# Kernel optimization log

Hardware: AMD Instinct MI355X
Metric: run time of the kernel (lower is better)

## Reference

```python
import math
import jax, jax.numpy as jnp
import numpy as np

BLOCK = 256
LAYER_IDX = 5
NUM_HIDDEN_LAYERS = 32


def get_slopes(head_dim):
    equ = lambda x: 1 / 2 ** (8 / x)
    log2 = math.log2(head_dim)
    if log2.is_integer():
        return [equ(head_dim) ** i for i in range(1, head_dim + 1)]
    lower = 2 ** math.floor(log2)
    upper = 2 ** math.ceil(log2)
    ls = get_slopes(lower)
    us = get_slopes(upper)
    return ls + us[::2][: head_dim - lower]


def setup_inputs() -> dict:
    key = jax.random.key(0)
    k1, k2, k3 = jax.random.split(key, 3)
    B, H, S, D = 2, 64, 4096, 64
    q = jax.random.normal(k1, (B, H, S, D), dtype=jnp.float32)
    k = jax.random.normal(k2, (B, H, S, D), dtype=jnp.float32)
    v = jax.random.normal(k3, (B, H, S, D), dtype=jnp.float32)
    mask = jnp.ones((B, S), dtype=jnp.int32)
    return {"query_states": q, "key_states": k, "value_states": v, "attention_mask": mask}


def _lightning_attention(q, k, v, attention_mask):
    B, H, S, D = q.shape
    E = v.shape[-1]
    # mask padded positions in values
    v = v * attention_mask[:, None, :, None].astype(v.dtype)

    # per-head decay slopes, scaled by layer depth (note: H == D by construction)
    slopes = np.asarray(get_slopes(D), dtype=np.float32)
    slopes = slopes * (1.0 - LAYER_IDX / (NUM_HIDDEN_LAYERS - 1) + 1e-05)
    slope = jnp.asarray(slopes)[:, None, None]  # [H, 1, 1]

    arr = jnp.arange(1, BLOCK + 1, dtype=jnp.float32)
    q_decay = jnp.exp(-slope * arr[:, None])            # [H, BLOCK, 1]
    k_decay = jnp.exp(-slope * (BLOCK - arr)[:, None])  # [H, BLOCK, 1]
    idx = arr[:, None] - arr[None, :]                   # [BLOCK, BLOCK]
    s_idx = slope * idx[None]                           # [H, BLOCK, BLOCK] (slope [H,1,1] broadcasts)
    diag_decay = jnp.exp(jnp.where(idx[None] >= 0, -s_idx, -jnp.inf))  # [H, BLOCK, BLOCK]
    block_decay = jnp.exp(-slope * BLOCK)               # [H, 1, 1]

    nb = S // BLOCK
    qb = q.reshape(B, H, nb, BLOCK, D).transpose(2, 0, 1, 3, 4)  # [nb, B, H, BLOCK, D]
    kb = k.reshape(B, H, nb, BLOCK, D).transpose(2, 0, 1, 3, 4)
    vb = v.reshape(B, H, nb, BLOCK, E).transpose(2, 0, 1, 3, 4)

    def step(kv, blk):
        qi, ki, vi = blk  # each [B, H, BLOCK, D/E]
        # inter-block: decayed query reads recurrent kv state
        o_inter = jnp.einsum('bhmd,bhde->bhme', qi * q_decay, kv)
        # intra-block: causal decayed attention within the block
        qk = jnp.einsum('bhmd,bhnd->bhmn', qi, ki) * diag_decay
        o_intra = jnp.einsum('bhmn,bhne->bhme', qk, vi)
        # update recurrent state
        kv_new = block_decay * kv + jnp.einsum('bhmd,bhme->bhde', ki * k_decay, vi)
        return kv_new, o_inter + o_intra

    kv0 = jnp.zeros((B, H, D, E), dtype=jnp.float32)
    _, outs = jax.lax.scan(step, kv0, (qb, kb, vb))  # outs: [nb, B, H, BLOCK, E]
    out = outs.transpose(1, 2, 0, 3, 4).reshape(B, H, S, E)
    return out


def reference(query_states, key_states, value_states, attention_mask):
    return _lightning_attention(query_states, key_states, value_states, attention_mask)
```

## Files before the change

### kernel.cpp

```cpp
#include <hip/hip_runtime.h>

typedef __attribute__((ext_vector_type(4))) float f4;
typedef __attribute__((ext_vector_type(4))) float f32x4;
typedef __attribute__((ext_vector_type(8))) short short8;
typedef __attribute__((ext_vector_type(4))) short short4v;
typedef __attribute__((ext_vector_type(4))) unsigned int uint4v;

#define S_  4096
#define NB_ 16
#define SLOPE_SCALE 0.838719677419355f

__device__ __forceinline__ float slope_for_head(int h) {
    return exp2f(-(float)(h + 1) * 0.125f) * SLOPE_SCALE;
}

__device__ __forceinline__ short f2bf(float f) {
    unsigned u = __float_as_uint(f);
    u += 0x7FFFu + ((u >> 16) & 1u);
    return (short)(u >> 16);
}

__global__ __launch_bounds__(256, 4) void phase1_kvblocks(
    const float* __restrict__ k, const float* __restrict__ v,
    const int* __restrict__ mask, float* __restrict__ kvt,
    short* __restrict__ vt)
{
    __shared__ float ks[64][68];
    __shared__ float vs[64][68];
    const int j  = blockIdx.x;
    const int bh = blockIdx.y;
    const int b  = bh >> 6;
    const int h  = bh & 63;
    const int t  = threadIdx.x;
    const float slope = slope_for_head(h);
    const int e  = t >> 2;
    const int dg = (t & 3) << 4;

    const f32x4 zf = {0.f, 0.f, 0.f, 0.f};
    f4 acc[4];
    acc[0] = zf; acc[1] = zf; acc[2] = zf; acc[3] = zf;

    const long long tilebase = ((long long)bh * S_ + j * 256) * 64;

    for (int c = 0; c < 4; ++c) {
        for (int i = 0; i < 4; ++i) {
            int fi  = t + i * 256;
            int row = fi >> 4;
            int col = (fi & 15) << 2;
            long long g = tilebase + (long long)(c * 64 + row) * 64 + col;
            *(f4*)&ks[row][col] = *(const f4*)(k + g);
            f4 vv = *(const f4*)(v + g);
            float mv = (float)mask[b * S_ + j * 256 + c * 64 + row];
            vv *= mv;
            *(f4*)&vs[row][col] = vv;
        }
        __syncthreads();

        for (int n = 0; n < 64; ++n) {
            float kd = __expf(-slope * (float)(255 - (c * 64 + n)));
            float a  = vs[n][e] * kd;
            const f4* krow = (const f4*)&ks[n][dg];
            acc[0] += a * krow[0];
            acc[1] += a * krow[1];
            acc[2] += a * krow[2];
            acc[3] += a * krow[3];
        }

        {
            int nb = (t & 3) << 4;
            unsigned w[8];
            for (int i = 0; i < 8; ++i) {
                unsigned lo = (unsigned short)f2bf(vs[nb + 2 * i][e]);
                unsigned hi = (unsigned short)f2bf(vs[nb + 2 * i + 1][e]);
                w[i] = lo | (hi << 16);
            }
            long long g = ((long long)(bh * 64 + e)) * S_ + j * 256 + c * 64 + nb;
            uint4v* dst = (uint4v*)(vt + g);
            uint4v w0 = {w[0], w[1], w[2], w[3]};
            uint4v w1 = {w[4], w[5], w[6], w[7]};
            dst[0] = w0;
            dst[1] = w1;
        }
        __syncthreads();
    }

    float* o = kvt + ((long long)(bh * NB_ + j)) * 4096 + e * 64 + dg;
    *(f4*)(o + 0)  = acc[0];
    *(f4*)(o + 4)  = acc[1];
    *(f4*)(o + 8)  = acc[2];
    *(f4*)(o + 12) = acc[3];
}

__global__ __launch_bounds__(256) void phase2_scan(float* __restrict__ kvt)
{
    const int bh = blockIdx.x;
    const int h  = bh & 63;
    const int t  = threadIdx.x;
    const float slope = slope_for_head(h);
    const float bd = __expf(-slope * 256.0f);

    const f32x4 zf = {0.f, 0.f, 0.f, 0.f};
    f4 st[4];
    st[0] = zf; st[1] = zf; st[2] = zf; st[3] = zf;

    f4* base = (f4*)(kvt + (long long)bh * NB_ * 4096);
    for (int j = 0; j < NB_; ++j) {
        f4* p = base + j * 1024;
        for (int i = 0; i < 4; ++i) {
            f4 tmp = p[t + i * 256];
            p[t + i * 256] = st[i];
            st[i] = st[i] * bd + tmp;
        }
    }
}

__global__ __launch_bounds__(256, 2) void phase3_output(
    const float* __restrict__ q, const float* __restrict__ k,
    const float* __restrict__ kvt, const short* __restrict__ vt,
    float* __restrict__ out)
{
    __shared__ short P[4][64 * 56];
    const int j    = blockIdx.x;
    const int bh   = blockIdx.y;
    const int h    = bh & 63;
    const int tid  = threadIdx.x;
    const int wave = tid >> 6;
    const int lane = tid & 63;
    const int quad = lane >> 4;
    const int l16  = lane & 15;
    const int wrole  = (wave + j) & 3;
    const float slope = slope_for_head(h);
    const int mwbase = wrole << 6;

    const long long rowbase = (long long)bh * S_ + j * 256 + mwbase;

    short8 qf[4][2];
    for (int mt = 0; mt < 4; ++mt) {
        const float* qp = q + (rowbase + mt * 16 + l16) * 64 + quad * 8;
        for (int ks = 0; ks < 2; ++ks) {
            f4 a = *(const f4*)(qp + ks * 32);
            f4 b = *(const f4*)(qp + ks * 32 + 4);
            short8 f;
            f[0] = f2bf(a.x); f[1] = f2bf(a.y); f[2] = f2bf(a.z); f[3] = f2bf(a.w);
            f[4] = f2bf(b.x); f[5] = f2bf(b.y); f[6] = f2bf(b.z); f[7] = f2bf(b.w);
            qf[mt][ks] = f;
        }
    }

    const f32x4 zf = {0.f, 0.f, 0.f, 0.f};
    f32x4 of[4][4];
    for (int et = 0; et < 4; ++et)
        for (int mt = 0; mt < 4; ++mt) of[et][mt] = zf;

    const float* kvp = kvt + ((long long)(bh * NB_ + j) << 12);
    for (int et = 0; et < 4; ++et) {
        for (int ks = 0; ks < 2; ++ks) {
            const float* p = kvp + (et * 16 + l16) * 64 + ks * 32 + quad * 8;
            f4 a = *(const f4*)(p);
            f4 b = *(const f4*)(p + 4);
            short8 af;
            af[0] = f2bf(a.x); af[1] = f2bf(a.y); af[2] = f2bf(a.z); af[3] = f2bf(a.w);
            af[4] = f2bf(b.x); af[5] = f2bf(b.y); af[6] = f2bf(b.z); af[7] = f2bf(b.w);
            for (int mt = 0; mt < 4; ++mt)
                of[et][mt] = __builtin_amdgcn_mfma_f32_16x16x32_bf16(
                    af, qf[mt][ks], of[et][mt], 0, 0, 0);
        }
    }
    for (int mt = 0; mt < 4; ++mt) {
        float qd = __expf(-slope * (float)(mwbase + mt * 16 + l16 + 1));
        for (int et = 0; et < 4; ++et) of[et][mt] *= qd;
    }

    const float er1 = __expf(slope);
    const float er2 = er1 * er1;
    const float er3 = er2 * er1;
    short* Pw = &P[wave][0];
    const int nchunks = (mwbase >> 5) + 2;

    for (int c = 0; c < nchunks; ++c) {
        const int nbase = c << 5;

        short8 kf[2][2];
        for (int nt = 0; nt < 2; ++nt) {
            const float* kp = k + ((long long)bh * S_ + j * 256 + nbase + nt * 16 + l16) * 64 + quad * 8;
            for (int ks = 0; ks < 2; ++ks) {
                f4 a = *(const f4*)(kp + ks * 32);
                f4 b = *(const f4*)(kp + ks * 32 + 4);
                short8 f;
                f[0] = f2bf(a.x); f[1] = f2bf(a.y); f[2] = f2bf(a.z); f[3] = f2bf(a.w);
                f[4] = f2bf(b.x); f[5] = f2bf(b.y); f[6] = f2bf(b.z); f[7] = f2bf(b.w);
                kf[nt][ks] = f;
            }
        }

        f32x4 sf[2][4];
        for (int nt = 0; nt < 2; ++nt)
            for (int mt = 0; mt < 4; ++mt) sf[nt][mt] = zf;
        for (int nt = 0; nt < 2; ++nt)
            for (int ks = 0; ks < 2; ++ks)
                for (int mt = 0; mt < 4; ++mt)
                    sf[nt][mt] = __builtin_amdgcn_mfma_f32_16x16x32_bf16(
                        kf[nt][ks], qf[mt][ks], sf[nt][mt], 0, 0, 0);

        for (int nt = 0; nt < 2; ++nt) {
            for (int mt = 0; mt < 4; ++mt) {
                int n0 = nbase + nt * 16 + quad * 4;
                int m  = mwbase + mt * 16 + l16;
                float ddb = __expf(-slope * (float)(m - n0));
                f32x4 s = sf[nt][mt];
                float v0 = (m >= n0)     ? s[0] * ddb       : 0.f;
                float v1 = (m >= n0 + 1) ? s[1] * ddb * er1 : 0.f;
                float v2 = (m >= n0 + 2) ? s[2] * ddb * er2 : 0.f;
                float v3 = (m >= n0 + 3) ? s[3] * ddb * er3 : 0.f;
                short4v pk = {f2bf(v0), f2bf(v1), f2bf(v2), f2bf(v3)};
                *(short4v*)&Pw[(mt * 16 + l16) * 56 + nt * 16 + quad * 4] = pk;
            }
        }
        asm volatile("s_waitcnt lgkmcnt(0)" ::: "memory");

        short8 pb[4];
        for (int mt = 0; mt < 4; ++mt)
            pb[mt] = *(const short8*)&Pw[(mt * 16 + l16) * 56 + quad * 8];
        short8 va[4];
        for (int et = 0; et < 4; ++et)
            va[et] = *(const short8*)(vt + ((long long)(bh * 64 + et * 16 + l16)) * S_
                                         + j * 256 + nbase + quad * 8);

        for (int et = 0; et < 4; ++et)
            for (int mt = 0; mt < 4; ++mt)
                of[et][mt] = __builtin_amdgcn_mfma_f32_16x16x32_bf16(
                    va[et], pb[mt], of[et][mt], 0, 0, 0);
    }

    for (int mt = 0; mt < 4; ++mt) {
        float* orow = out + (rowbase + mt * 16 + l16) * 64;
        for (int et = 0; et < 4; ++et) {
            f4 o = {of[et][mt][0], of[et][mt][1], of[et][mt][2], of[et][mt][3]};
            *(f4*)(orow + et * 16 + quad * 4) = o;
        }
    }
}

extern "C" void kernel_launch(void* const* d_in, const int* in_sizes, int n_in,
                              void* d_out, int out_size, void* d_ws, size_t ws_size,
                              hipStream_t stream) {
    const float* q    = (const float*)d_in[0];
    const float* k    = (const float*)d_in[1];
    const float* v    = (const float*)d_in[2];
    const int*   mask = (const int*)d_in[3];
    float* kvt = (float*)d_ws;
    short* vt  = (short*)((char*)d_ws + (size_t)128 * 16 * 4096 * 4);
    float* out = (float*)d_out;

    phase1_kvblocks<<<dim3(16, 128), 256, 0, stream>>>(k, v, mask, kvt, vt);
    phase2_scan<<<128, 256, 0, stream>>>(kvt);
    phase3_output<<<dim3(16, 128), 256, 0, stream>>>(q, k, kvt, vt, out);
}
```

Baseline: 552.1 us.

## Use MFMA for block KV state, precompute bf16 K, and widen scan grid

```diff
diff --git a/kernel.cpp b/kernel.cpp
--- a/kernel.cpp
+++ b/kernel.cpp
@@ -4,11 +4,11 @@
 typedef __attribute__((ext_vector_type(4))) float f32x4;
 typedef __attribute__((ext_vector_type(8))) short short8;
 typedef __attribute__((ext_vector_type(4))) short short4v;
-typedef __attribute__((ext_vector_type(4))) unsigned int uint4v;
 
 #define S_  4096
 #define NB_ 16
 #define SLOPE_SCALE 0.838719677419355f
+#define ST1 136
 
 __device__ __forceinline__ float slope_for_head(int h) {
     return exp2f(-(float)(h + 1) * 0.125f) * SLOPE_SCALE;
@@ -23,99 +23,111 @@
 __global__ __launch_bounds__(256, 4) void phase1_kvblocks(
     const float* __restrict__ k, const float* __restrict__ v,
     const int* __restrict__ mask, float* __restrict__ kvt,
-    short* __restrict__ vt)
+    short* __restrict__ vt, short* __restrict__ kb)
 {
-    __shared__ float ks[64][68];
-    __shared__ float vs[64][68];
-    const int j  = blockIdx.x;
-    const int bh = blockIdx.y;
-    const int b  = bh >> 6;
-    const int h  = bh & 63;
-    const int t  = threadIdx.x;
+    __shared__ short kts[64 * ST1];
+    __shared__ short vts[64 * ST1];
+    const int j    = blockIdx.x;
+    const int bh   = blockIdx.y;
+    const int b    = bh >> 6;
+    const int h    = bh & 63;
+    const int t    = threadIdx.x;
+    const int wave = t >> 6;
+    const int lane = t & 63;
+    const int quad = lane >> 4;
+    const int l16  = lane & 15;
     const float slope = slope_for_head(h);
-    const int e  = t >> 2;
-    const int dg = (t & 3) << 4;
+
+    const long long tilebase = ((long long)bh * S_ + j * 256) * 64;
 
     const f32x4 zf = {0.f, 0.f, 0.f, 0.f};
-    f4 acc[4];
+    f32x4 acc[4];
     acc[0] = zf; acc[1] = zf; acc[2] = zf; acc[3] = zf;
 
-    const long long tilebase = ((long long)bh * S_ + j * 256) * 64;
-
-    for (int c = 0; c < 4; ++c) {
+    for (int half = 0; half < 2; ++half) {
+        const int noff = half * 128;
+
         for (int i = 0; i < 4; ++i) {
-            int fi  = t + i * 256;
-            int row = fi >> 4;
-            int col = (fi & 15) << 2;
-            long long g = tilebase + (long long)(c * 64 + row) * 64 + col;
-            *(f4*)&ks[row][col] = *(const f4*)(k + g);
-            f4 vv = *(const f4*)(v + g);
-            float mv = (float)mask[b * S_ + j * 256 + c * 64 + row];
-            vv *= mv;
-            *(f4*)&vs[row][col] = vv;
+            int u  = t + i * 256;
+            int np = u >> 4;
+            int dg = (u & 15) << 2;
+            int nl = np << 1;
+            int na = noff + nl;
+            long long g0 = tilebase + (long long)na * 64 + dg;
+
+            f4 k0 = *(const f4*)(k + g0);
+            f4 k1 = *(const f4*)(k + g0 + 64);
+            f4 v0 = *(const f4*)(v + g0);
+            f4 v1 = *(const f4*)(v + g0 + 64);
+            float m0 = (float)mask[b * S_ + j * 256 + na];
+            float m1 = (float)mask[b * S_ + j * 256 + na + 1];
+            v0 *= m0; v1 *= m1;
+            float kd0 = __expf(-slope * (float)(255 - na));
+            float kd1 = __expf(-slope * (float)(254 - na));
+
+            short4v kb0 = {f2bf(k0.x), f2bf(k0.y), f2bf(k0.z), f2bf(k0.w)};
+            short4v kb1 = {f2bf(k1.x), f2bf(k1.y), f2bf(k1.z), f2bf(k1.w)};
+            *(short4v*)(kb + g0) = kb0;
+            *(short4v*)(kb + g0 + 64) = kb1;
+
+            f4 kda = k0 * kd0;
+            f4 kdb = k1 * kd1;
+            for (int x = 0; x < 4; ++x) {
+                unsigned kw = (unsigned)(unsigned short)f2bf(kda[x]) |
+                              ((unsigned)(unsigned short)f2bf(kdb[x]) << 16);
+                unsigned vw = (unsigned)(unsigned short)f2bf(v0[x]) |
+                              ((unsigned)(unsigned short)f2bf(v1[x]) << 16);
+                *(unsigned*)&kts[(dg + x) * ST1 + nl] = kw;
+                *(unsigned*)&vts[(dg + x) * ST1 + nl] = vw;
+            }
         }
         __syncthreads();
 
-        for (int n = 0; n < 64; ++n) {
-            float kd = __expf(-slope * (float)(255 - (c * 64 + n)));
-            float a  = vs[n][e] * kd;
-            const f4* krow = (const f4*)&ks[n][dg];
-            acc[0] += a * krow[0];
-            acc[1] += a * krow[1];
-            acc[2] += a * krow[2];
-            acc[3] += a * krow[3];
+        for (int ks = 0; ks < 4; ++ks) {
+            int n0 = ks * 32;
+            short8 af = *(const short8*)&vts[(wave * 16 + l16) * ST1 + n0 + quad * 8];
+            for (int dt = 0; dt < 4; ++dt) {
+                short8 bf = *(const short8*)&kts[(dt * 16 + l16) * ST1 + n0 + quad * 8];
+                acc[dt] = __builtin_amdgcn_mfma_f32_16x16x32_bf16(af, bf, acc[dt], 0, 0, 0);
+            }
         }
 
         {
-            int nb = (t & 3) << 4;
-            unsigned w[8];
-            for (int i = 0; i < 8; ++i) {
-                unsigned lo = (unsigned short)f2bf(vs[nb + 2 * i][e]);
-                unsigned hi = (unsigned short)f2bf(vs[nb + 2 * i + 1][e]);
-                w[i] = lo | (hi << 16);
-            }
-            long long g = ((long long)(bh * 64 + e)) * S_ + j * 256 + c * 64 + nb;
-            uint4v* dst = (uint4v*)(vt + g);
-            uint4v w0 = {w[0], w[1], w[2], w[3]};
-            uint4v w1 = {w[4], w[5], w[6], w[7]};
-            dst[0] = w0;
-            dst[1] = w1;
+            int e  = t >> 2;
+            int ng = (t & 3) << 5;
+            long long gv = (long long)(bh * 64 + e) * S_ + j * 256 + noff + ng;
+            for (int x = 0; x < 4; ++x)
+                *(short8*)(vt + gv + x * 8) = *(const short8*)&vts[e * ST1 + ng + x * 8];
         }
         __syncthreads();
     }
 
-    float* o = kvt + ((long long)(bh * NB_ + j)) * 4096 + e * 64 + dg;
-    *(f4*)(o + 0)  = acc[0];
-    *(f4*)(o + 4)  = acc[1];
-    *(f4*)(o + 8)  = acc[2];
-    *(f4*)(o + 12) = acc[3];
+    float* o = kvt + ((long long)(bh * NB_ + j)) * 4096;
+    for (int dt = 0; dt < 4; ++dt)
+        for (int r = 0; r < 4; ++r)
+            o[(wave * 16 + quad * 4 + r) * 64 + dt * 16 + l16] = acc[dt][r];
 }
 
 __global__ __launch_bounds__(256) void phase2_scan(float* __restrict__ kvt)
 {
-    const int bh = blockIdx.x;
-    const int h  = bh & 63;
-    const int t  = threadIdx.x;
-    const float slope = slope_for_head(h);
-    const float bd = __expf(-slope * 256.0f);
-
-    const f32x4 zf = {0.f, 0.f, 0.f, 0.f};
-    f4 st[4];
-    st[0] = zf; st[1] = zf; st[2] = zf; st[3] = zf;
-
-    f4* base = (f4*)(kvt + (long long)bh * NB_ * 4096);
+    const int g    = blockIdx.x;
+    const int bh   = g >> 2;
+    const int part = g & 3;
+    const int h    = bh & 63;
+    const float bd = __expf(-slope_for_head(h) * 256.0f);
+
+    f32x4 st = {0.f, 0.f, 0.f, 0.f};
+    f4* base = (f4*)(kvt + (long long)bh * NB_ * 4096) + part * 256 + threadIdx.x;
     for (int j = 0; j < NB_; ++j) {
         f4* p = base + j * 1024;
-        for (int i = 0; i < 4; ++i) {
-            f4 tmp = p[t + i * 256];
-            p[t + i * 256] = st[i];
-            st[i] = st[i] * bd + tmp;
-        }
-    }
-}
-
-__global__ __launch_bounds__(256, 2) void phase3_output(
-    const float* __restrict__ q, const float* __restrict__ k,
+        f4 tmp = *p;
+        *p = st;
+        st = st * bd + tmp;
+    }
+}
+
+__global__ __launch_bounds__(256, 4) void phase3_output(
+    const float* __restrict__ q, const short* __restrict__ kb,
     const float* __restrict__ kvt, const short* __restrict__ vt,
     float* __restrict__ out)
 {
@@ -182,15 +194,9 @@
 
         short8 kf[2][2];
         for (int nt = 0; nt < 2; ++nt) {
-            const float* kp = k + ((long long)bh * S_ + j * 256 + nbase + nt * 16 + l16) * 64 + quad * 8;
-            for (int ks = 0; ks < 2; ++ks) {
-                f4 a = *(const f4*)(kp + ks * 32);
-                f4 b = *(const f4*)(kp + ks * 32 + 4);
-                short8 f;
-                f[0] = f2bf(a.x); f[1] = f2bf(a.y); f[2] = f2bf(a.z); f[3] = f2bf(a.w);
-                f[4] = f2bf(b.x); f[5] = f2bf(b.y); f[6] = f2bf(b.z); f[7] = f2bf(b.w);
-                kf[nt][ks] = f;
-            }
+            const short* kp = kb + ((long long)bh * S_ + j * 256 + nbase + nt * 16 + l16) * 64 + quad * 8;
+            kf[nt][0] = *(const short8*)(kp);
+            kf[nt][1] = *(const short8*)(kp + 32);
         }
 
         f32x4 sf[2][4];
@@ -250,9 +256,10 @@
     const int*   mask = (const int*)d_in[3];
     float* kvt = (float*)d_ws;
     short* vt  = (short*)((char*)d_ws + (size_t)128 * 16 * 4096 * 4);
+    short* kb  = (short*)((char*)vt + (size_t)128 * 4096 * 64 * 2);
     float* out = (float*)d_out;
 
-    phase1_kvblocks<<<dim3(16, 128), 256, 0, stream>>>(k, v, mask, kvt, vt);
-    phase2_scan<<<128, 256, 0, stream>>>(kvt);
-    phase3_output<<<dim3(16, 128), 256, 0, stream>>>(q, k, kvt, vt, out);
-}
+    phase1_kvblocks<<<dim3(16, 128), 256, 0, stream>>>(k, v, mask, kvt, vt, kb);
+    phase2_scan<<<512, 256, 0, stream>>>(kvt);
+    phase3_output<<<dim3(16, 128), 256, 0, stream>>>(q, kb, kvt, vt, out);
+}
```

Result: slower. 697.8 us (+26.4%).
